# Kernel tuning notes

Hardware: AMD Instinct MI355X
Metric: run time of the kernel (lower is better)

Reference implementation:

```python
import jax, jax.numpy as jnp
import numpy as np
import math

PI = math.pi
POS_RANGE = (0.0, PI, -PI, PI)            # (x_lo, x_hi, y_lo, y_hi)
DIR_RANGE = (0.5 * PI, 0.85 * PI, -0.85 * PI, -0.5 * PI)


def setup_inputs() -> dict:
    key = jax.random.key(0)
    kx, kg, kw1, kw2 = jax.random.split(key, 4)
    N = 1_048_576
    G0, G1, G2, G3, F = 64, 64, 32, 32, 16
    # sample query points strictly inside the valid angular ranges
    lo = jnp.array([POS_RANGE[0], POS_RANGE[2], DIR_RANGE[0], DIR_RANGE[2]], jnp.float32)
    hi = jnp.array([POS_RANGE[1], POS_RANGE[3], DIR_RANGE[1], DIR_RANGE[3]], jnp.float32)
    u = jax.random.uniform(kx, (N, 4), jnp.float32, 0.0, 0.999)
    x = lo + u * (hi - lo)
    # xavier-uniform learned 4D feature grid
    gb = math.sqrt(6.0 / (G3 + F))
    grid = jax.random.uniform(kg, (G0, G1, G2, G3, F), jnp.float32, -gb, gb)
    H = 4 * F
    b1v = math.sqrt(6.0 / (F + H))
    w1 = jax.random.uniform(kw1, (F, H), jnp.float32, -b1v, b1v)
    b1 = jnp.zeros((H,), jnp.float32)
    b2v = math.sqrt(6.0 / (H + 3))
    w2 = jax.random.uniform(kw2, (H, 3), jnp.float32, -b2v, b2v)
    b2 = jnp.zeros((3,), jnp.float32)
    return {"x": x, "grid": grid, "w1": w1, "b1": b1, "w2": w2, "b2": b2}


def _quadlinear(x, grid):
    G0, G1, G2, G3, F = grid.shape
    # normalize each coordinate to grid index space (faithful to original,
    # including normalizing dim0 by G0-1 / dim1 by G1-1 while dim0 indexes axis 1)
    c0 = (x[:, 0] - POS_RANGE[0]) / (POS_RANGE[1] - POS_RANGE[0]) * (G0 - 1)
    c1 = (x[:, 1] - POS_RANGE[2]) / (POS_RANGE[3] - POS_RANGE[2]) * (G1 - 1)
    c2 = (x[:, 2] - DIR_RANGE[0]) / (DIR_RANGE[1] - DIR_RANGE[0]) * (G2 - 1)
    c3 = (x[:, 3] - DIR_RANGE[2]) / (DIR_RANGE[3] - DIR_RANGE[2]) * (G3 - 1)
    W, H, D, T = G1 - 1, G0 - 1, G2 - 1, G3 - 1
    tlx = c0.astype(jnp.int32)  # coords are non-negative -> trunc == floor
    tly = c1.astype(jnp.int32)
    tlz = c2.astype(jnp.int32)
    tlw = c3.astype(jnp.int32)
    xf = jnp.mod(c0, 1.0)[:, None]
    yf = jnp.mod(c1, 1.0)[:, None]
    zf = jnp.mod(c2, 1.0)[:, None]
    wf = jnp.mod(c3, 1.0)[:, None]
    brx = jnp.minimum(tlx + 1, W)
    bry = jnp.minimum(tly + 1, H)
    brz = jnp.minimum(tlz + 1, D)
    brw = jnp.minimum(tlw + 1, T)
    g = lambda a, b, c, d: grid[a, b, c, d]  # [N, F] gather
    c0000 = g(tly, tlx, tlz, tlw); c1000 = g(tly, brx, tlz, tlw)
    c0100 = g(bry, tlx, tlz, tlw); c0010 = g(tly, tlx, brz, tlw)
    c0001 = g(tly, tlx, tlz, brw); c1100 = g(bry, brx, tlz, tlw)
    c1010 = g(tly, brx, brz, tlw); c1001 = g(tly, brx, tlz, brw)
    c0110 = g(bry, tlx, brz, tlw); c0101 = g(bry, tlx, tlz, brw)
    c0011 = g(tly, tlx, brz, brw); c1110 = g(bry, brx, brz, tlw)
    c1101 = g(bry, brx, tlz, brw); c1011 = g(tly, brx, brz, brw)
    c0111 = g(bry, tlx, brz, brw); c1111 = g(bry, brx, brz, brw)
    c00 = c0000 * (1 - xf) + c1000 * xf
    c01 = c0001 * (1 - xf) + c1001 * xf
    c10 = c0100 * (1 - xf) + c1100 * xf
    c11 = c0110 * (1 - xf) + c1110 * xf
    c20 = c0010 * (1 - xf) + c1010 * xf
    c21 = c0011 * (1 - xf) + c1011 * xf
    c30 = c0101 * (1 - xf) + c1101 * xf
    c31 = c0111 * (1 - xf) + c1111 * xf
    cc0 = c00 * (1 - yf) + c10 * yf
    cc1 = c01 * (1 - yf) + c11 * yf
    cc2 = c20 * (1 - yf) + c30 * yf
    cc3 = c21 * (1 - yf) + c31 * yf
    c4 = cc0 * (1 - zf) + cc2 * zf
    c5 = cc1 * (1 - zf) + cc3 * zf
    return c4 * (1 - wf) + c5 * wf  # [N, F]


def reference(x, grid, w1, b1, w2, b2):
    feat = _quadlinear(x, grid)
    h = feat @ w1 + b1
    h = jnp.where(h >= 0, h, 0.01 * h)  # LeakyReLU(0.01)
    out = h @ w2 + b2
    return jax.nn.sigmoid(out) * 255.0
```

## Files before the change

### kernel.cpp

```cpp
#include <hip/hip_runtime.h>
#include <math.h>


#define NBUCKET 131072
#define SCAN_BLOCKS 128
#define FEAT_PITCH 260

__device__ __forceinline__ int point_key(const float4 xv) {
    const float c0 = xv.x * (63.0f / (float)M_PI);
    const float c1 = (xv.y + (float)M_PI) * (63.0f / (float)(2.0 * M_PI));
    const float c2 = (xv.z - (float)(0.5 * M_PI)) * (31.0f / (float)(0.35 * M_PI));
    int tx = min(max((int)c0, 0), 63);
    int ty = min(max((int)c1, 0), 63);
    int tz = min(max((int)c2, 0), 31);
    return (ty * 64 + tx) * 32 + tz;
}

__global__ __launch_bounds__(1024) void k_zero(unsigned* __restrict__ hist) {
    hist[blockIdx.x * 1024 + threadIdx.x] = 0u;
}

__global__ __launch_bounds__(256) void k_hist(const float4* __restrict__ x,
                                              unsigned* __restrict__ hist, int N) {
    const int p = blockIdx.x * 256 + threadIdx.x;
    if (p >= N) return;
    atomicAdd(&hist[point_key(x[p])], 1u);
}

__global__ __launch_bounds__(1024) void k_scanA(unsigned* __restrict__ data,
                                                unsigned* __restrict__ partial) {
    __shared__ unsigned s[1024];
    const int t = threadIdx.x;
    const int base = blockIdx.x * 1024;
    const unsigned v = data[base + t];
    s[t] = v;
    __syncthreads();
    #pragma unroll
    for (int off = 1; off < 1024; off <<= 1) {
        const unsigned add = (t >= off) ? s[t - off] : 0u;
        __syncthreads();
        s[t] += add;
        __syncthreads();
    }
    data[base + t] = (t == 0) ? 0u : s[t - 1];
    if (t == 1023) partial[blockIdx.x] = s[1023];
}

__global__ __launch_bounds__(SCAN_BLOCKS) void k_scanB(unsigned* __restrict__ partial) {
    __shared__ unsigned s[SCAN_BLOCKS];
    const int t = threadIdx.x;
    const unsigned v = partial[t];
    s[t] = v;
    __syncthreads();
    #pragma unroll
    for (int off = 1; off < SCAN_BLOCKS; off <<= 1) {
        const unsigned add = (t >= off) ? s[t - off] : 0u;
        __syncthreads();
        s[t] += add;
        __syncthreads();
    }
    partial[t] = s[t] - v;
}

__global__ __launch_bounds__(1024) void k_scanC(unsigned* __restrict__ data,
                                                const unsigned* __restrict__ partial) {
    data[blockIdx.x * 1024 + threadIdx.x] += partial[blockIdx.x];
}

__global__ __launch_bounds__(256) void k_scatter(const float4* __restrict__ x,
                                                 unsigned* __restrict__ offsets,
                                                 float4* __restrict__ xs,
                                                 unsigned* __restrict__ idx, int N) {
    const int p = blockIdx.x * 256 + threadIdx.x;
    if (p >= N) return;
    const float4 xv = x[p];
    const unsigned slot = atomicAdd(&offsets[point_key(xv)], 1u);
    xs[slot] = xv;
    idx[slot] = p;
}

template <bool SORTED>
__global__ __launch_bounds__(256, 4) void gridnet_main(
    const float4* __restrict__ xs,
    const unsigned* __restrict__ idx,
    const float* __restrict__ grid,
    const float* __restrict__ w1, const float* __restrict__ b1,
    const float* __restrict__ w2, const float* __restrict__ b2,
    float* __restrict__ out, int N, int nblk)
{
    __shared__ float w1s[1024];
    __shared__ float featS[16 * FEAT_PITCH];
    __shared__ float b1s[64];
    __shared__ float w2s[192];
    __shared__ float b2s[4];

    const int t = threadIdx.x;
    for (int i = t; i < 1024; i += 256) w1s[i] = w1[i];
    if (t < 64)  b1s[t] = b1[t];
    if (t < 192) w2s[t] = w2[t];
    if (t < 3)   b2s[t] = b2[t];

    int b = blockIdx.x;
    if ((nblk & 7) == 0)
        b = (blockIdx.x & 7) * (nblk >> 3) + (blockIdx.x >> 3);
    const int base = b * 256;

    const float lo1 = (float)(-M_PI);
    const float sp0 = (float)(M_PI);
    const float sp1 = (float)(2.0 * M_PI);
    const float lo2 = (float)(0.5 * M_PI);
    const float sp2 = (float)(0.85 * M_PI - 0.5 * M_PI);
    const float lo3 = (float)(-0.85 * M_PI);
    const float sp3 = (float)(-0.5 * M_PI - (-0.85 * M_PI));

    const int l  = t & 3;
    const int qb = t >> 2;

    #pragma unroll
    for (int k = 0; k < 4; ++k) {
        const int pl = qb + 64 * k;
        const int gp = base + pl;
        float4 acc = make_float4(0.f, 0.f, 0.f, 0.f);
        if (gp < N) {
            const float4 xv = xs[gp];

            const float c0 = (xv.x - 0.0f) / sp0 * 63.0f;
            const float c1 = (xv.y - lo1) / sp1 * 63.0f;
            const float c2 = (xv.z - lo2) / sp2 * 31.0f;
            const float c3 = (xv.w - lo3) / sp3 * 31.0f;

            const int tlx = (int)c0;
            const int tly = (int)c1;
            const int tlz = (int)c2;
            const int tlw = (int)c3;

            const float xf = c0 - (float)tlx;
            const float yf = c1 - (float)tly;
            const float zf = c2 - (float)tlz;
            const float wf = c3 - (float)tlw;

            const int brx = min(tlx + 1, 63);
            const int bry = min(tly + 1, 63);
            const int brz = min(tlz + 1, 31);
            const int brw = min(tlw + 1, 31);

            const float wx0 = 1.0f - xf, wx1 = xf;
            const float wy0 = 1.0f - yf, wy1 = yf;
            const float wz0 = 1.0f - zf, wz1 = zf;
            const float ww0 = 1.0f - wf, ww1 = wf;

            float cw[2][2][2];
            cw[0][0][0] = wy0 * wz0 * ww0;
            cw[0][0][1] = wy0 * wz0 * ww1;
            cw[0][1][0] = wy0 * wz1 * ww0;
            cw[0][1][1] = wy0 * wz1 * ww1;
            cw[1][0][0] = wy1 * wz0 * ww0;
            cw[1][0][1] = wy1 * wz1 * ww0;
            cw[1][1][0] = wy1 * wz0 * ww1;
            cw[1][1][1] = wy1 * wz1 * ww1;

            const float wxv[2] = {wx0, wx1};
            const int axv[2] = {tlx, brx};
            const int ayv[2] = {tly, bry};
            const int azv[2] = {tlz, brz};
            const int awv[2] = {tlw, brw};

            float wk[16];
            int   ofs[16];
            #pragma unroll
            for (int iy = 0; iy < 2; ++iy)
              #pragma unroll
              for (int ix = 0; ix < 2; ++ix) {
                const int base1 = (ayv[iy] * 64 + axv[ix]) * 32;
                #pragma unroll
                for (int iz = 0; iz < 2; ++iz) {
                  const int base0 = (base1 + azv[iz]) * 32;
                  #pragma unroll
                  for (int iw = 0; iw < 2; ++iw) {
                    const int kk = ((iy * 2 + ix) * 2 + iz) * 2 + iw;
                    wk[kk]  = wxv[ix] * cw[iy][iz][iw];
                    ofs[kk] = (base0 + awv[iw]) * 64 + l * 16;
                  }
                }
              }

            #pragma unroll
            for (int h8 = 0; h8 < 2; ++h8) {
                float4 cv[8];
                #pragma unroll
                for (int c = 0; c < 8; ++c)
                    cv[c] = *reinterpret_cast<const float4*>(
                        reinterpret_cast<const char*>(grid) + ofs[h8 * 8 + c]);
                #pragma unroll
                for (int c = 0; c < 8; ++c) {
                    const float w = wk[h8 * 8 + c];
                    acc.x += w * cv[c].x;
                    acc.y += w * cv[c].y;
                    acc.z += w * cv[c].z;
                    acc.w += w * cv[c].w;
                }
            }
        }
        featS[(4 * l + 0) * FEAT_PITCH + pl] = acc.x;
        featS[(4 * l + 1) * FEAT_PITCH + pl] = acc.y;
        featS[(4 * l + 2) * FEAT_PITCH + pl] = acc.z;
        featS[(4 * l + 3) * FEAT_PITCH + pl] = acc.w;
    }
    __syncthreads();

    const int g  = t & 7;
    const int pg = t >> 3;

    float h[8][8];
    #pragma unroll
    for (int p = 0; p < 8; ++p)
        #pragma unroll
        for (int j = 0; j < 8; ++j)
            h[p][j] = b1s[g * 8 + j];

    #pragma unroll
    for (int i = 0; i < 16; ++i) {
        const float4 wA = *reinterpret_cast<const float4*>(&w1s[i * 64 + g * 8]);
        const float4 wB = *reinterpret_cast<const float4*>(&w1s[i * 64 + g * 8 + 4]);
        const float4 fA = *reinterpret_cast<const float4*>(&featS[i * FEAT_PITCH + pg * 8]);
        const float4 fB = *reinterpret_cast<const float4*>(&featS[i * FEAT_PITCH + pg * 8 + 4]);
        const float fv[8] = {fA.x, fA.y, fA.z, fA.w, fB.x, fB.y, fB.z, fB.w};
        const float wv[8] = {wA.x, wA.y, wA.z, wA.w, wB.x, wB.y, wB.z, wB.w};
        #pragma unroll
        for (int p = 0; p < 8; ++p)
            #pragma unroll
            for (int j = 0; j < 8; ++j)
                h[p][j] += fv[p] * wv[j];
    }

    float o[8][3];
    #pragma unroll
    for (int p = 0; p < 8; ++p) { o[p][0] = 0.f; o[p][1] = 0.f; o[p][2] = 0.f; }

    #pragma unroll
    for (int j = 0; j < 8; ++j) {
        const float w20 = w2s[(g * 8 + j) * 3 + 0];
        const float w21 = w2s[(g * 8 + j) * 3 + 1];
        const float w22 = w2s[(g * 8 + j) * 3 + 2];
        #pragma unroll
        for (int p = 0; p < 8; ++p) {
            const float hv = (h[p][j] >= 0.0f) ? h[p][j] : 0.01f * h[p][j];
            o[p][0] += hv * w20;
            o[p][1] += hv * w21;
            o[p][2] += hv * w22;
        }
    }

    #pragma unroll
    for (int m = 1; m < 8; m <<= 1)
        #pragma unroll
        for (int p = 0; p < 8; ++p) {
            o[p][0] += __shfl_xor(o[p][0], m);
            o[p][1] += __shfl_xor(o[p][1], m);
            o[p][2] += __shfl_xor(o[p][2], m);
        }

    float og[3];
    #pragma unroll
    for (int p = 0; p < 8; ++p)
        if (p == g) { og[0] = o[p][0]; og[1] = o[p][1]; og[2] = o[p][2]; }

    const int pl = pg * 8 + g;
    const int gp = base + pl;
    if (gp < N) {
        const int op = SORTED ? (int)idx[gp] : gp;
        float* dst = out + (size_t)op * 3;
        #pragma unroll
        for (int c = 0; c < 3; ++c) {
            const float v = og[c] + b2s[c];
            dst[c] = 255.0f / (1.0f + expf(-v));
        }
    }
}

extern "C" void kernel_launch(void* const* d_in, const int* in_sizes, int n_in,
                              void* d_out, int out_size, void* d_ws, size_t ws_size,
                              hipStream_t stream) {
    const float* x    = (const float*)d_in[0];
    const float* grid = (const float*)d_in[1];
    const float* w1   = (const float*)d_in[2];
    const float* b1   = (const float*)d_in[3];
    const float* w2   = (const float*)d_in[4];
    const float* b2   = (const float*)d_in[5];
    float* out = (float*)d_out;

    const int N = in_sizes[0] / 4;
    const int nblk = (N + 255) / 256;

    const size_t xs_bytes   = (size_t)N * 16;
    const size_t idx_bytes  = (size_t)N * 4;
    const size_t hist_bytes = (size_t)NBUCKET * 4;
    const size_t part_bytes = (size_t)SCAN_BLOCKS * 4;
    const size_t need = xs_bytes + idx_bytes + hist_bytes + part_bytes;

    if (ws_size >= need) {
        char* ws = (char*)d_ws;
        float4*   xs      = (float4*)ws;
        unsigned* idx     = (unsigned*)(ws + xs_bytes);
        unsigned* hist    = (unsigned*)(ws + xs_bytes + idx_bytes);
        unsigned* partial = (unsigned*)(ws + xs_bytes + idx_bytes + hist_bytes);
        const float4* x4 = (const float4*)x;

        k_zero   <<<NBUCKET / 1024, 1024, 0, stream>>>(hist);
        k_hist   <<<nblk, 256, 0, stream>>>(x4, hist, N);
        k_scanA  <<<SCAN_BLOCKS, 1024, 0, stream>>>(hist, partial);
        k_scanB  <<<1, SCAN_BLOCKS, 0, stream>>>(partial);
        k_scanC  <<<SCAN_BLOCKS, 1024, 0, stream>>>(hist, partial);
        k_scatter<<<nblk, 256, 0, stream>>>(x4, hist, xs, idx, N);
        gridnet_main<true><<<nblk, 256, 0, stream>>>(
            xs, idx, grid, w1, b1, w2, b2, out, N, nblk);
    } else {
        gridnet_main<false><<<nblk, 256, 0, stream>>>(
            (const float4*)x, nullptr, grid, w1, b1, w2, b2, out, N, nblk);
    }
}
```

Measured before the change: 299.4 us.

## Sort query points by 4D Morton key including coarse w dimension

Changes the bucket key used to sort points before the main gather kernel. It moves from a 3D row-major key to a 21-bit Morton (Z-order) key over y, x, z and a halved w coordinate, so points that land in the same gather neighborhood are grouped more tightly and cache reuse of grid corners improves. The bucket count grows from 131072 to 2 million, so the histogram, scans and memset handle 16x more data. The second-level scan is reworked to process 2048 partials, and the zeroing kernel is replaced by hipMemsetAsync.

New measurement: 325.8 us. 8.8% more time.

```diff
diff --git a/kernel.cpp b/kernel.cpp
--- a/kernel.cpp
+++ b/kernel.cpp
@@ -2,22 +2,33 @@
 #include <math.h>
 
 
-#define NBUCKET 131072
-#define SCAN_BLOCKS 128
+#define NBUCKET (1u << 21)
+#define SCAN_BLOCKS 2048
 #define FEAT_PITCH 260
 
-__device__ __forceinline__ int point_key(const float4 xv) {
+__device__ __forceinline__ unsigned morton_key(int ty, int tx, int tz, int tw2) {
+    unsigned k = 0;
+    int pos = 0;
+    #pragma unroll
+    for (int b = 0; b < 6; ++b) {
+        if (b < 4) { k |= ((unsigned)((tw2 >> b) & 1)) << pos; ++pos; }
+        if (b < 5) { k |= ((unsigned)((tz  >> b) & 1)) << pos; ++pos; }
+        k |= ((unsigned)((tx >> b) & 1)) << pos; ++pos;
+        k |= ((unsigned)((ty >> b) & 1)) << pos; ++pos;
+    }
+    return k;
+}
+
+__device__ __forceinline__ unsigned point_key(const float4 xv) {
     const float c0 = xv.x * (63.0f / (float)M_PI);
     const float c1 = (xv.y + (float)M_PI) * (63.0f / (float)(2.0 * M_PI));
     const float c2 = (xv.z - (float)(0.5 * M_PI)) * (31.0f / (float)(0.35 * M_PI));
+    const float c3 = (xv.w + (float)(0.85 * M_PI)) * (31.0f / (float)(0.35 * M_PI));
     int tx = min(max((int)c0, 0), 63);
     int ty = min(max((int)c1, 0), 63);
     int tz = min(max((int)c2, 0), 31);
-    return (ty * 64 + tx) * 32 + tz;
-}
-
-__global__ __launch_bounds__(1024) void k_zero(unsigned* __restrict__ hist) {
-    hist[blockIdx.x * 1024 + threadIdx.x] = 0u;
+    int tw = min(max((int)c3, 0), 31);
+    return morton_key(ty, tx, tz, tw >> 1);
 }
 
 __global__ __launch_bounds__(256) void k_hist(const float4* __restrict__ x,
@@ -46,20 +57,23 @@
     if (t == 1023) partial[blockIdx.x] = s[1023];
 }
 
-__global__ __launch_bounds__(SCAN_BLOCKS) void k_scanB(unsigned* __restrict__ partial) {
-    __shared__ unsigned s[SCAN_BLOCKS];
+__global__ __launch_bounds__(1024) void k_scanB(unsigned* __restrict__ partial) {
+    __shared__ unsigned s[1024];
     const int t = threadIdx.x;
-    const unsigned v = partial[t];
-    s[t] = v;
+    const unsigned v0 = partial[2 * t];
+    const unsigned v1 = partial[2 * t + 1];
+    s[t] = v0 + v1;
     __syncthreads();
     #pragma unroll
-    for (int off = 1; off < SCAN_BLOCKS; off <<= 1) {
+    for (int off = 1; off < 1024; off <<= 1) {
         const unsigned add = (t >= off) ? s[t - off] : 0u;
         __syncthreads();
         s[t] += add;
         __syncthreads();
     }
-    partial[t] = s[t] - v;
+    const unsigned exc = (t == 0) ? 0u : s[t - 1];
+    partial[2 * t] = exc;
+    partial[2 * t + 1] = exc + v0;
 }
 
 __global__ __launch_bounds__(1024) void k_scanC(unsigned* __restrict__ data,
@@ -306,10 +320,10 @@
         unsigned* partial = (unsigned*)(ws + xs_bytes + idx_bytes + hist_bytes);
         const float4* x4 = (const float4*)x;
 
-        k_zero   <<<NBUCKET / 1024, 1024, 0, stream>>>(hist);
+        hipMemsetAsync(hist, 0, hist_bytes, stream);
         k_hist   <<<nblk, 256, 0, stream>>>(x4, hist, N);
         k_scanA  <<<SCAN_BLOCKS, 1024, 0, stream>>>(hist, partial);
-        k_scanB  <<<1, SCAN_BLOCKS, 0, stream>>>(partial);
+        k_scanB  <<<1, 1024, 0, stream>>>(partial);
         k_scanC  <<<SCAN_BLOCKS, 1024, 0, stream>>>(hist, partial);
         k_scatter<<<nblk, 256, 0, stream>>>(x4, hist, xs, idx, N);
         gridnet_main<true><<<nblk, 256, 0, stream>>>(
```
